# Optimization experiments

Measured on AMD Instinct MI355X. Metric: run time of the kernel, lower is better.

The kernel has to match this reference:

```python
import jax, jax.numpy as jnp
import numpy as np

EPS = 1e-5
BS, NA, NC, NL, NPTS, ED, NG = 1, 900, 6, 4, 13, 256, 8
GD = ED // NG
IMG_W, IMG_H = 704.0, 256.0
FMAP_HW = [(64, 176), (32, 88), (16, 44), (8, 22)]


def _ln(x, g, b):
    m = x.mean(-1, keepdims=True)
    v = ((x - m) ** 2).mean(-1, keepdims=True)
    return (x - m) / jnp.sqrt(v + EPS) * g + b


def _grid_sample(img, grid):
    # img: [N,C,H,W]; grid: [N,P,Q,2] in [-1,1]; bilinear, zeros padding, align_corners=False
    N, C, H, W = img.shape
    gx = jnp.clip((grid[..., 0] + 1.0) * (W * 0.5) - 0.5, -1e4, 1e4)
    gy = jnp.clip((grid[..., 1] + 1.0) * (H * 0.5) - 0.5, -1e4, 1e4)
    x0 = jnp.floor(gx); y0 = jnp.floor(gy)
    wx1 = gx - x0; wy1 = gy - y0; wx0 = 1.0 - wx1; wy0 = 1.0 - wy1
    x0i = x0.astype(jnp.int32); y0i = y0.astype(jnp.int32)
    flat = img.reshape(N, C, H * W)

    def corner(xi, yi, wgt):
        valid = (xi >= 0) & (xi < W) & (yi >= 0) & (yi < H)
        idx = (jnp.clip(yi, 0, H - 1) * W + jnp.clip(xi, 0, W - 1))
        g = jax.vmap(lambda f, i: f[:, i])(flat, idx.reshape(N, -1))  # [N,C,P*Q]
        g = g.reshape(N, C, idx.shape[1], idx.shape[2])
        return g * (wgt * valid)[:, None]

    return (corner(x0i, y0i, wx0 * wy0) + corner(x0i + 1, y0i, wx1 * wy0)
            + corner(x0i, y0i + 1, wx0 * wy1) + corner(x0i + 1, y0i + 1, wx1 * wy1))


def setup_inputs() -> dict:
    key = jax.random.key(0)
    ks = jax.random.split(key, 20)
    d = {}
    d['instance_feature'] = jax.random.normal(ks[0], (BS, NA, ED), jnp.float32)
    xyz = jax.random.normal(ks[1], (BS, NA, 3), jnp.float32) * 1.5
    size = jax.random.normal(ks[2], (BS, NA, 3), jnp.float32) * 0.3
    theta = jax.random.uniform(ks[3], (BS, NA, 1), jnp.float32) * (2.0 * np.pi)
    vel = jax.random.normal(ks[4], (BS, NA, 3), jnp.float32) * 0.1
    d['anchor'] = jnp.concatenate([xyz, size, jnp.sin(theta), jnp.cos(theta), vel], -1)
    d['anchor_embed'] = jax.random.normal(ks[5], (BS, NA, ED), jnp.float32)
    for i, (h, w) in enumerate(FMAP_HW):
        d[f'fmap{i}'] = jax.random.normal(ks[6 + i], (BS, NC, ED, h, w), jnp.float32)
    base = jnp.array([[80., 0., 0., 352.], [0., 80., 0., 128.],
                      [0., 0., 0., 1.], [0., 0., 0., 1.]], jnp.float32)
    proj = jnp.tile(base, (BS, NC, 1, 1))
    proj = proj.at[:, :, :2, :].add(jax.random.normal(ks[10], (BS, NC, 2, 4), jnp.float32) * 2.0)
    d['projection_mat'] = proj
    d['image_wh'] = jnp.broadcast_to(jnp.array([IMG_W, IMG_H], jnp.float32), (BS, NC, 2))
    d['fix_scale'] = jnp.array([[0, 0, 0], [0.45, 0, 0], [-0.45, 0, 0], [0, 0.45, 0],
                                [0, -0.45, 0], [0, 0, 0.45], [0, 0, -0.45]], jnp.float32)

    def w(k, shape):
        return jax.random.normal(k, shape, jnp.float32) * 0.02

    d['lfc_w'] = w(ks[11], (ED, 6 * 3)); d['lfc_b'] = jnp.zeros((18,), jnp.float32)
    d['cam_w1'] = w(ks[12], (12, ED)); d['cam_b1'] = jnp.zeros((ED,), jnp.float32)
    d['cam_g1'] = jnp.ones((ED,), jnp.float32); d['cam_be1'] = jnp.zeros((ED,), jnp.float32)
    d['cam_w2'] = w(ks[13], (ED, ED)); d['cam_b2'] = jnp.zeros((ED,), jnp.float32)
    d['cam_g2'] = jnp.ones((ED,), jnp.float32); d['cam_be2'] = jnp.zeros((ED,), jnp.float32)
    d['wfc_w'] = w(ks[14], (ED, NG * NL * NPTS)); d['wfc_b'] = jnp.zeros((NG * NL * NPTS,), jnp.float32)
    d['op_w'] = w(ks[15], (ED, ED)); d['op_b'] = jnp.zeros((ED,), jnp.float32)
    return d


def reference(instance_feature, anchor, anchor_embed, fmap0, fmap1, fmap2, fmap3,
              projection_mat, image_wh, fix_scale, lfc_w, lfc_b,
              cam_w1, cam_b1, cam_g1, cam_be1, cam_w2, cam_b2, cam_g2, cam_be2,
              wfc_w, wfc_b, op_w, op_b):
    bs, na = instance_feature.shape[:2]
    # ---- keypoint generation ----
    size = jnp.exp(anchor[..., None, 3:6])                       # [bs,na,1,3]
    kp = fix_scale * size                                        # [bs,na,7,3]
    ls = jax.nn.sigmoid(instance_feature @ lfc_w + lfc_b).reshape(bs, na, -1, 3) - 0.5
    kp = jnp.concatenate([kp, ls * size], axis=-2)               # [bs,na,NPTS,3]
    sin, cos = anchor[..., 6:7], anchor[..., 7:8]                # [bs,na,1]
    kx, ky, kz = kp[..., 0], kp[..., 1], kp[..., 2]
    key_points = jnp.stack([cos * kx - sin * ky, sin * kx + cos * ky, kz], -1) \
                 + anchor[..., None, 0:3]                        # [bs,na,NPTS,3]
    # ---- per-cam/level/point group weights ----
    feat = instance_feature + anchor_embed
    cam_in = projection_mat[:, :, :3].reshape(bs, NC, 12)
    h = jax.nn.relu(cam_in @ cam_w1 + cam_b1); h = _ln(h, cam_g1, cam_be1)
    h = jax.nn.relu(h @ cam_w2 + cam_b2); cam_embed = _ln(h, cam_g2, cam_be2)
    f = feat[:, :, None] + cam_embed[:, None]                    # [bs,na,NC,ED]
    wts = (f @ wfc_w + wfc_b).reshape(bs, na, NC * NL * NPTS, NG)
    wts = jax.nn.softmax(wts, axis=-2).reshape(bs, na, NC, NL, NPTS, NG)
    # ---- multi-cam projection + bilinear sampling ----
    pts = jnp.concatenate([key_points, jnp.ones_like(key_points[..., :1])], -1)
    p2d = jnp.einsum('bcij,banj->bcani', projection_mat, pts)    # [bs,NC,na,NPTS,4]
    p2d = p2d[..., :2] / jnp.maximum(p2d[..., 2:3], 1e-5)
    p2d = p2d / image_wh[:, :, None, None]
    grid = (p2d * 2.0 - 1.0).reshape(bs * NC, na, NPTS, 2)
    feats = jnp.stack([_grid_sample(fm.reshape(bs * NC, ED, fm.shape[-2], fm.shape[-1]), grid)
                       for fm in (fmap0, fmap1, fmap2, fmap3)], axis=1)  # [bs*NC,NL,ED,na,NPTS]
    feats = feats.reshape(bs, NC, NL, ED, na, NPTS).transpose(0, 4, 1, 2, 5, 3)  # [bs,na,NC,NL,NPTS,ED]
    # ---- group-weighted fusion over cams & levels, then sum over points ----
    fg = feats.reshape(bs, na, NC, NL, NPTS, NG, GD)
    fused = jnp.einsum('bnclpg,bnclpgd->bnpgd', wts, fg).reshape(bs, na, NPTS, ED)
    fused = fused.sum(axis=2)                                    # [bs,na,ED]
    out = fused @ op_w + op_b
    return jnp.concatenate([out, instance_feature], axis=-1)     # [bs,na,2*ED]
```

## Files before the change

### kernel.cpp

```cpp
#include <hip/hip_runtime.h>
#include <stdint.h>

#define NA 900
#define NC 6
#define NL 4
#define NPTS 13
#define ED 256
#define NG 8
#define LNEPS 1e-5f
#define NTRANS 1416
#define NCOPY 672
#define NSAMP 312
#define LGS 313

struct PIn { const void* p[24]; };

__device__ __forceinline__ float b2f(unsigned short u){
  union { uint32_t i; float f; } v; v.i = ((uint32_t)u)<<16; return v.f;
}
__device__ __forceinline__ unsigned short f2b(float f){
  union { float f; uint32_t i; } v; v.f = f;
  uint32_t r = v.i + 0x7FFFu + ((v.i>>16)&1u);
  return (unsigned short)(r>>16);
}
#define BLO(u) __uint_as_float((u)<<16)
#define BHI(u) __uint_as_float((u)&0xffff0000u)

__device__ __forceinline__ float ldx(const void* p, int i, bool bf){
  return bf ? b2f(((const unsigned short*)p)[i]) : ((const float*)p)[i];
}

__device__ __forceinline__ void gload_lds16(const void* g, void* l){
  __builtin_amdgcn_global_load_lds(
      (const __attribute__((address_space(1))) void*)g,
      (__attribute__((address_space(3))) void*)l, 16, 0, 0);
}

__device__ __forceinline__ bool sniff_bf(const unsigned short* __restrict__ u16){
  int lane = threadIdx.x & 63;
  unsigned short u = u16[2*lane];
  int e = (u>>7)&0xFF;
  int sane = (e>=110 && e<=135) ? 1 : 0;
  #pragma unroll
  for (int m=32;m;m>>=1) sane += __shfl_xor(sane, m);
  return sane >= 48;
}

__device__ __forceinline__ void blockReduce2(float& a, float& b, float* lds){
  #pragma unroll
  for (int m=32;m;m>>=1){ a += __shfl_xor(a,m); b += __shfl_xor(b,m); }
  int w = threadIdx.x>>6;
  if ((threadIdx.x&63)==0){ lds[w]=a; lds[w+4]=b; }
  __syncthreads();
  a = lds[0]+lds[1]+lds[2]+lds[3];
  b = lds[4]+lds[5]+lds[6]+lds[7];
  __syncthreads();
}

__global__ __launch_bounds__(256) void k_init(PIn in,
                                              unsigned short* __restrict__ wfcw_h,
                                              unsigned short* __restrict__ opw_h,
                                              float* __restrict__ Bc){
  const bool bf = sniff_bf((const unsigned short*)in.p[0]);
  const int tid = threadIdx.x;
  int b = blockIdx.x;

  __shared__ float h[ED];
  __shared__ float cE[ED];
  __shared__ float red8[8];
  __shared__ float part[4][64];

  if (b < NCOPY){
    int idx = b*256 + tid;
    if (idx < 106496){
      wfcw_h[idx] = bf ? ((const unsigned short*)in.p[20])[idx]
                       : f2b(((const float*)in.p[20])[idx]);
    } else {
      int j = idx - 106496;
      opw_h[j] = bf ? ((const unsigned short*)in.p[22])[j]
                    : f2b(((const float*)in.p[22])[j]);
    }
    return;
  }
  b -= NCOPY;
  {
    const void* proj = in.p[7];
    const void* w1 = in.p[12]; const void* b1 = in.p[13];
    const void* g1 = in.p[14]; const void* be1 = in.p[15];
    const void* w2 = in.p[16]; const void* b2 = in.p[17];
    const void* g2 = in.p[18]; const void* be2 = in.p[19];
    const void* wfcw = in.p[20]; const void* wfcb = in.p[21];
    const int c = b/7, colt = b - (b/7)*7;
    float ci[12];
    #pragma unroll
    for (int i=0;i<12;i++) ci[i] = ldx(proj, c*16+i, bf);
    float acc = ldx(b1, tid, bf);
    #pragma unroll
    for (int k=0;k<12;k++) acc += ci[k]*ldx(w1, k*ED+tid, bf);
    float x = fmaxf(acc, 0.f);
    float s=x, q=x*x;
    blockReduce2(s,q,red8);
    float mean = s*(1.f/ED), var = q*(1.f/ED)-mean*mean;
    h[tid] = (x-mean)*rsqrtf(var+LNEPS)*ldx(g1,tid,bf) + ldx(be1,tid,bf);
    __syncthreads();
    acc = ldx(b2, tid, bf);
    #pragma unroll 8
    for (int k=0;k<ED;k++) acc += h[k]*ldx(w2, k*ED+tid, bf);
    x = fmaxf(acc,0.f);
    s=x; q=x*x;
    blockReduce2(s,q,red8);
    mean = s*(1.f/ED); var = q*(1.f/ED)-mean*mean;
    cE[tid] = (x-mean)*rsqrtf(var+LNEPS)*ldx(g2,tid,bf) + ldx(be2,tid,bf);
    __syncthreads();
    const int kc = tid>>6, colL = tid&63, col = colt*64+colL;
    float a = 0.f;
    if (col < 416){
      #pragma unroll 8
      for (int k=0;k<64;k++) a += cE[kc*64+k]*ldx(wfcw, (kc*64+k)*416+col, bf);
    }
    part[kc][colL] = a;
    __syncthreads();
    if (kc==0 && col<416)
      Bc[c*416+col] = part[0][colL]+part[1][colL]+part[2][colL]+part[3][colL] + ldx(wfcb,col,bf);
  }
}

__global__ __launch_bounds__(256) void k_work(PIn in,
                                              unsigned short* __restrict__ tf,
                                              const unsigned short* __restrict__ wfcw_h,
                                              const float* __restrict__ Bc,
                                              uint4* __restrict__ gdesc, int* __restrict__ mcnt,
                                              void* __restrict__ outv){
  const bool bf = sniff_bf((const unsigned short*)in.p[0]);
  const int tid = threadIdx.x;
  int b = blockIdx.x;

  __shared__ __align__(16) char smem[32768];

  if (b < NTRANS){
    const int tiles[4] = {44,11,3,1};
    const int HWs[4]   = {11264,2816,704,176};
    const int TFO[4]   = {0,17301504,21626880,22708224};
    int l, local;
    if      (b < 1056){ l=0; local=b;      }
    else if (b < 1320){ l=1; local=b-1056; }
    else if (b < 1392){ l=2; local=b-1320; }
    else              { l=3; local=b-1392; }
    int pt = local % tiles[l]; int rest = local / tiles[l];
    int ct = rest & 3; int c = rest >> 2;
    const int HW = HWs[l];
    const int px0 = pt*256;
    const void* src = in.p[3+l];
    const int j8 = tid & 7;
    const int w8 = tid >> 3;

    int nq = 4;
    while (nq > 1 && px0 + (nq-1)*64 >= HW) nq--;

    if (!bf){
      float* TTf = (float*)smem;
      const int wv = tid >> 6;
      const int ln = tid & 63;
      const int rq = ln >> 4;
      const int g  = ln & 15;

      auto issueph = [&](int q){
        const int pxq = px0 + q*64;
        float* dst0 = TTf + (q&1)*4096;
        #pragma unroll
        for (int i=0;i<4;i++){
          int r   = wv*16 + i*4 + rq;
          int swz = (r>>3) & 7;
          int px  = pxq + 4*(g ^ swz);
          if (px + 4 > HW) px = HW - 4;
          const float* gsrc = (const float*)src + (size_t)(c*ED + ct*64 + r)*HW + px;
          gload_lds16(gsrc, (void*)(dst0 + (wv*16 + i*4)*64));
        }
      };

      issueph(0);
      for (int q=0; q<nq; q++){
        if (q+1 < nq){
          issueph(q+1);
          asm volatile("s_waitcnt vmcnt(4)" ::: "memory");
        } else {
          asm volatile("s_waitcnt vmcnt(0)" ::: "memory");
        }
        __builtin_amdgcn_s_barrier();
        const float* T = TTf + (q&1)*4096;
        #pragma unroll
        for (int p=0;p<2;p++){
          int pxl = p*32 + w8;
          int px  = px0 + q*64 + pxl;
          int s   = 4*((pxl>>2) ^ j8) + (pxl&3);
          if (px < HW){
            unsigned short u[8];
            #pragma unroll
            for (int k=0;k<8;k++)
              u[k] = f2b(T[(j8*8+k)*64 + s]);
            uint4 o;
            o.x = (uint32_t)u[0] | ((uint32_t)u[1]<<16);
            o.y = (uint32_t)u[2] | ((uint32_t)u[3]<<16);
            o.z = (uint32_t)u[4] | ((uint32_t)u[5]<<16);
            o.w = (uint32_t)u[6] | ((uint32_t)u[7]<<16);
            *reinterpret_cast<uint4*>(tf + TFO[l] + (size_t)c*HW*ED + (size_t)px*ED + ct*64 + j8*8) = o;
          }
        }
        __builtin_amdgcn_s_barrier();
      }
      return;
    }
    {
      typedef unsigned short u16tile[64][64];
      u16tile* TT = (u16tile*)smem;
      uint4 v[2][4];
      #pragma unroll
      for (int p=0;p<2;p++){
        int ch = ct*64 + p*32 + w8;
        size_t rowb = (size_t)(c*ED+ch)*HW;
        #pragma unroll
        for (int q=0;q<4;q++){
          int pxs = px0 + q*64 + j8*8;
          v[p][q] = (pxs < HW)
            ? *reinterpret_cast<const uint4*>((const unsigned short*)src + rowb + pxs)
            : make_uint4(0,0,0,0);
        }
      }
      for (int q=0;q<nq;q++){
        const int buf = q & 1;
        #pragma unroll
        for (int p=0;p<2;p++){
          int r = p*32 + w8;
          int g8 = (j8 ^ (r>>3))<<3;
          *reinterpret_cast<uint4*>(&TT[buf][r][g8]) = v[p][q];
        }
        __syncthreads();
        #pragma unroll
        for (int p=0;p<2;p++){
          int pxl = p*32 + w8;
          int px  = px0 + q*64 + pxl;
          int colq = (((pxl>>3) ^ j8)<<3) | (pxl & 7);
          int rb = j8*8;
          unsigned short t0 = TT[buf][rb+0][colq], t1 = TT[buf][rb+1][colq];
          unsigned short t2 = TT[buf][rb+2][colq], t3 = TT[buf][rb+3][colq];
          unsigned short t4 = TT[buf][rb+4][colq], t5 = TT[buf][rb+5][colq];
          unsigned short t6 = TT[buf][rb+6][colq], t7 = TT[buf][rb+7][colq];
          uint4 o;
          o.x = (uint32_t)t0 | ((uint32_t)t1<<16);
          o.y = (uint32_t)t2 | ((uint32_t)t3<<16);
          o.z = (uint32_t)t4 | ((uint32_t)t5<<16);
          o.w = (uint32_t)t6 | ((uint32_t)t7<<16);
          if (px < HW)
            *reinterpret_cast<uint4*>(tf + TFO[l] + (size_t)c*HW*ED + (size_t)px*ED + ct*64 + j8*8) = o;
        }
      }
      return;
    }
  }
  const int n = b - NTRANS;
  float* ifs = (float*)(smem);
  float* fe  = (float*)(smem + 1024);
  float* lg2 = (float*)(smem + 2048);
  float (*kp)[3] = (float (*)[3])(smem + 12160);
  float* sc  = (float*)(smem + 12352);
  float* lsv = (float*)(smem + 12416);
  int*   scnt= (int*)(smem + 12544);

  const void* p_inst = in.p[0];
  const void* p_anc  = in.p[1];
  const void* p_ae   = in.p[2];
  const void* p_proj = in.p[7];
  const void* p_imwh = in.p[8];
  const void* p_fixs = in.p[9];
  const void* p_lw   = in.p[10];
  const void* p_lb   = in.p[11];

  {
    if (tid==0) *scnt = 0;
    float iv = ldx(p_inst, n*ED+tid, bf);
    ifs[tid] = iv;
    fe[tid]  = iv + ldx(p_ae, n*ED+tid, bf);
    if (bf) ((unsigned short*)outv)[n*512+256+tid] = f2b(iv);
    else    ((float*)outv)[n*512+256+tid]          = iv;
    if (tid >= 256-8){
      int t = tid - (256-8);
      if (t < 3)       sc[t] = ldx(p_anc, n*11+t, bf);
      else if (t == 3) sc[3] = ldx(p_anc, n*11+6, bf);
      else if (t == 4) sc[4] = ldx(p_anc, n*11+7, bf);
      else             sc[t] = __expf(ldx(p_anc, n*11+t-2, bf));
    }
  }
  __syncthreads();
  if (tid < 144){
    int d = tid>>3, j = tid&7;
    float a = 0.f;
    #pragma unroll 8
    for (int k=j*32;k<j*32+32;k++) a += ifs[k]*ldx(p_lw, k*18+d, bf);
    a += __shfl_xor(a,1); a += __shfl_xor(a,2); a += __shfl_xor(a,4);
    if (j==0){
      a += ldx(p_lb, d, bf);
      lsv[d] = 1.f/(1.f+__expf(-a)) - 0.5f;
    }
  }
  __syncthreads();
  if (tid < 13){
    float kx,ky,kz;
    if (tid < 7){
      kx = ldx(p_fixs, tid*3+0, bf)*sc[5];
      ky = ldx(p_fixs, tid*3+1, bf)*sc[6];
      kz = ldx(p_fixs, tid*3+2, bf)*sc[7];
    } else {
      int j = tid-7;
      kx = lsv[j*3+0]*sc[5]; ky = lsv[j*3+1]*sc[6]; kz = lsv[j*3+2]*sc[7];
    }
    kp[tid][0] = sc[4]*kx - sc[3]*ky + sc[0];
    kp[tid][1] = sc[3]*kx + sc[4]*ky + sc[1];
    kp[tid][2] = kz + sc[2];
  }
  {
    int col2 = (tid < 160) ? tid+256 : 415;
    float a0 = 0.f, a1 = 0.f;
    #pragma unroll 4
    for (int k=0;k<ED;k++){
      float fv = fe[k];
      a0 += fv*b2f(wfcw_h[k*416+tid]);
      a1 += fv*b2f(wfcw_h[k*416+col2]);
    }
    const int g = tid & 7, rr = tid >> 3;
    const int g2 = col2 & 7, rr2 = col2 >> 3;
    #pragma unroll
    for (int c=0;c<NC;c++){
      lg2[g*LGS + c*52 + rr] = a0 + Bc[c*416+tid];
      if (tid < 160) lg2[g2*LGS + c*52 + rr2] = a1 + Bc[c*416+col2];
    }
  }
  __syncthreads();
  {
    const int g = tid>>5, j = tid&31;
    float v[10]; float mx = -1e30f;
    #pragma unroll
    for (int i=0;i<10;i++){
      int e = j + 32*i;
      float val = -1e30f;
      if (e < NSAMP){ val = lg2[g*LGS + e]; mx = fmaxf(mx, val); }
      v[i] = val;
    }
    #pragma unroll
    for (int mk=16;mk;mk>>=1) mx = fmaxf(mx, __shfl_xor(mx, mk, 32));
    float sum = 0.f;
    #pragma unroll
    for (int i=0;i<10;i++){
      if (j + 32*i < NSAMP){ float ex = __expf(v[i]-mx); v[i] = ex; sum += ex; }
    }
    #pragma unroll
    for (int mk=16;mk;mk>>=1) sum += __shfl_xor(sum, mk, 32);
    float inv = 1.f/sum;
    #pragma unroll
    for (int i=0;i<10;i++){
      int e = j + 32*i;
      if (e < NSAMP) lg2[g*LGS + e] = v[i]*inv;
    }
  }
  __syncthreads();
  #pragma unroll
  for (int pass=0;pass<2;pass++){
    int s = tid + pass*256;
    if (s < NSAMP){
      int c = s/52, rr = s - c*52;
      int l = rr/13, p = rr - l*13;
      float m[12];
      #pragma unroll
      for (int i=0;i<12;i++) m[i] = ldx(p_proj, c*16+i, bf);
      float X=kp[p][0], Y=kp[p][1], Z=kp[p][2];
      float x = m[0]*X + m[1]*Y + m[2]*Z  + m[3];
      float y = m[4]*X + m[5]*Y + m[6]*Z  + m[7];
      float z = m[8]*X + m[9]*Y + m[10]*Z + m[11];
      float d = fmaxf(z, 1e-5f);
      float px = x/(d*ldx(p_imwh, c*2+0, bf)), py = y/(d*ldx(p_imwh, c*2+1, bf));
      const int W = 176>>l, H = 64>>l;
      const int TFO[4] = {0,17301504,21626880,22708224};
      float gx = fminf(fmaxf(px*(float)W - 0.5f, -10000.f), 10000.f);
      float gy = fminf(fmaxf(py*(float)H - 0.5f, -10000.f), 10000.f);
      float xf = floorf(gx), yf = floorf(gy);
      int x0 = (int)xf, y0 = (int)yf;
      float wx1 = gx-xf, wy1 = gy-yf;
      float wx0 = 1.f-wx1, wy0 = 1.f-wy1;
      bool vx0 = (x0>=0)&&(x0<W),   vx1 = (x0+1>=0)&&(x0+1<W);
      bool vy0 = (y0>=0)&&(y0<H),   vy1 = (y0+1>=0)&&(y0+1<H);
      float w00 = (vx0&&vy0) ? wx0*wy0 : 0.f;
      float w10 = (vx1&&vy0) ? wx1*wy0 : 0.f;
      float w01 = (vx0&&vy1) ? wx0*wy1 : 0.f;
      float w11 = (vx1&&vy1) ? wx1*wy1 : 0.f;
      if (w00+w10+w01+w11 != 0.f){
        int cx0 = min(max(x0,0),W-1), cx1 = min(max(x0+1,0),W-1);
        int cy0 = min(max(y0,0),H-1), cy1 = min(max(y0+1,0),H-1);
        uint32_t cam = (uint32_t)TFO[l] + (uint32_t)(c*H*W)*ED;
        uint4 bi, wv;
        bi.x = cam + (uint32_t)(cy0*W+cx0)*ED;
        bi.y = cam + (uint32_t)(cy0*W+cx1)*ED;
        bi.z = cam + (uint32_t)(cy1*W+cx0)*ED;
        bi.w = cam + (uint32_t)(cy1*W+cx1)*ED;
        wv.x = __float_as_uint(w00); wv.y = __float_as_uint(w10);
        wv.z = __float_as_uint(w01); wv.w = __float_as_uint(w11);
        float4 wa = make_float4(lg2[0*LGS+s], lg2[1*LGS+s], lg2[2*LGS+s], lg2[3*LGS+s]);
        float4 wb = make_float4(lg2[4*LGS+s], lg2[5*LGS+s], lg2[6*LGS+s], lg2[7*LGS+s]);
        int slot = atomicAdd(scnt, 1);
        uint4* dst = gdesc + (size_t)(n*NSAMP + slot)*4;
        dst[0] = bi;
        dst[1] = wv;
        dst[2] = *reinterpret_cast<uint4*>(&wa);
        dst[3] = *reinterpret_cast<uint4*>(&wb);
      }
    }
  }
  __syncthreads();
  if (tid==0) mcnt[n] = *scnt;
}

__global__ __launch_bounds__(512, 4) void k_gather(
    const unsigned short* __restrict__ tf,
    const unsigned short* __restrict__ opw_h, const uint4* __restrict__ gdesc,
    const int* __restrict__ mcnt, const void* __restrict__ rawinst,
    const void* __restrict__ opb, void* __restrict__ outv){
  const int n = blockIdx.x, tid = threadIdx.x;
  const bool bf = sniff_bf((const unsigned short*)rawinst);

  __shared__ uint4 ldesc[NSAMP*4];
  __shared__ float red[8][ED+4];
  __shared__ float fu[ED];

  const int m = mcnt[n];
  {
    const uint4* src = gdesc + (size_t)n*NSAMP*4;
    for (int j=tid; j < m*4; j += 512) ldesc[j] = src[j];
  }
  __syncthreads();

  {
    const int strm = tid>>5, lane32 = tid&31;
    const int ch8 = lane32*8, gg = lane32>>2;
    float acc[8] = {0,0,0,0,0,0,0,0};
    int i = strm;
    for (; i + 16 < m; i += 32){
      uint4 biA = ldesc[i*4],      wfA = ldesc[i*4+1];
      uint4 biB = ldesc[(i+16)*4], wfB = ldesc[(i+16)*4+1];
      float wgA = reinterpret_cast<const float*>(&ldesc[i*4+2])[gg];
      float wgB = reinterpret_cast<const float*>(&ldesc[(i+16)*4+2])[gg];
      uint4 a00 = *reinterpret_cast<const uint4*>(tf + biA.x + ch8);
      uint4 a10 = *reinterpret_cast<const uint4*>(tf + biA.y + ch8);
      uint4 a01 = *reinterpret_cast<const uint4*>(tf + biA.z + ch8);
      uint4 a11 = *reinterpret_cast<const uint4*>(tf + biA.w + ch8);
      uint4 b00 = *reinterpret_cast<const uint4*>(tf + biB.x + ch8);
      uint4 b10 = *reinterpret_cast<const uint4*>(tf + biB.y + ch8);
      uint4 b01 = *reinterpret_cast<const uint4*>(tf + biB.z + ch8);
      uint4 b11 = *reinterpret_cast<const uint4*>(tf + biB.w + ch8);
      float pA00 = wgA*__uint_as_float(wfA.x), pA10 = wgA*__uint_as_float(wfA.y);
      float pA01 = wgA*__uint_as_float(wfA.z), pA11 = wgA*__uint_as_float(wfA.w);
      float pB00 = wgB*__uint_as_float(wfB.x), pB10 = wgB*__uint_as_float(wfB.y);
      float pB01 = wgB*__uint_as_float(wfB.z), pB11 = wgB*__uint_as_float(wfB.w);
      acc[0] += pA00*BLO(a00.x)+pA10*BLO(a10.x)+pA01*BLO(a01.x)+pA11*BLO(a11.x)
              + pB00*BLO(b00.x)+pB10*BLO(b10.x)+pB01*BLO(b01.x)+pB11*BLO(b11.x);
      acc[1] += pA00*BHI(a00.x)+pA10*BHI(a10.x)+pA01*BHI(a01.x)+pA11*BHI(a11.x)
              + pB00*BHI(b00.x)+pB10*BHI(b10.x)+pB01*BHI(b01.x)+pB11*BHI(b11.x);
      acc[2] += pA00*BLO(a00.y)+pA10*BLO(a10.y)+pA01*BLO(a01.y)+pA11*BLO(a11.y)
              + pB00*BLO(b00.y)+pB10*BLO(b10.y)+pB01*BLO(b01.y)+pB11*BLO(b11.y);
      acc[3] += pA00*BHI(a00.y)+pA10*BHI(a10.y)+pA01*BHI(a01.y)+pA11*BHI(a11.y)
              + pB00*BHI(b00.y)+pB10*BHI(b10.y)+pB01*BHI(b01.y)+pB11*BHI(b11.y);
      acc[4] += pA00*BLO(a00.z)+pA10*BLO(a10.z)+pA01*BLO(a01.z)+pA11*BLO(a11.z)
              + pB00*BLO(b00.z)+pB10*BLO(b10.z)+pB01*BLO(b01.z)+pB11*BLO(b11.z);
      acc[5] += pA00*BHI(a00.z)+pA10*BHI(a10.z)+pA01*BHI(a01.z)+pA11*BHI(a11.z)
              + pB00*BHI(b00.z)+pB10*BHI(b10.z)+pB01*BHI(b01.z)+pB11*BHI(b11.z);
      acc[6] += pA00*BLO(a00.w)+pA10*BLO(a10.w)+pA01*BLO(a01.w)+pA11*BLO(a11.w)
              + pB00*BLO(b00.w)+pB10*BLO(b10.w)+pB01*BLO(b01.w)+pB11*BLO(b11.w);
      acc[7] += pA00*BHI(a00.w)+pA10*BHI(a10.w)+pA01*BHI(a01.w)+pA11*BHI(a11.w)
              + pB00*BHI(b00.w)+pB10*BHI(b10.w)+pB01*BHI(b01.w)+pB11*BHI(b11.w);
    }
    for (; i < m; i += 16){
      uint4 bi = ldesc[i*4], wf = ldesc[i*4+1];
      float wg = reinterpret_cast<const float*>(&ldesc[i*4+2])[gg];
      uint4 q00 = *reinterpret_cast<const uint4*>(tf + bi.x + ch8);
      uint4 q10 = *reinterpret_cast<const uint4*>(tf + bi.y + ch8);
      uint4 q01 = *reinterpret_cast<const uint4*>(tf + bi.z + ch8);
      uint4 q11 = *reinterpret_cast<const uint4*>(tf + bi.w + ch8);
      float p00 = wg*__uint_as_float(wf.x), p10 = wg*__uint_as_float(wf.y);
      float p01 = wg*__uint_as_float(wf.z), p11 = wg*__uint_as_float(wf.w);
      acc[0] += p00*BLO(q00.x)+p10*BLO(q10.x)+p01*BLO(q01.x)+p11*BLO(q11.x);
      acc[1] += p00*BHI(q00.x)+p10*BHI(q10.x)+p01*BHI(q01.x)+p11*BHI(q11.x);
      acc[2] += p00*BLO(q00.y)+p10*BLO(q10.y)+p01*BLO(q01.y)+p11*BLO(q11.y);
      acc[3] += p00*BHI(q00.y)+p10*BHI(q10.y)+p01*BHI(q01.y)+p11*BHI(q11.y);
      acc[4] += p00*BLO(q00.z)+p10*BLO(q10.z)+p01*BLO(q01.z)+p11*BLO(q11.z);
      acc[5] += p00*BHI(q00.z)+p10*BHI(q10.z)+p01*BHI(q01.z)+p11*BHI(q11.z);
      acc[6] += p00*BLO(q00.w)+p10*BLO(q10.w)+p01*BLO(q01.w)+p11*BLO(q11.w);
      acc[7] += p00*BHI(q00.w)+p10*BHI(q10.w)+p01*BHI(q01.w)+p11*BHI(q11.w);
    }
    #pragma unroll
    for (int j=0;j<8;j++) acc[j] += __shfl_xor(acc[j], 32);
    const int w = tid>>6;
    if ((tid&63) < 32){
      *reinterpret_cast<float4*>(&red[w][ch8])   = make_float4(acc[0],acc[1],acc[2],acc[3]);
      *reinterpret_cast<float4*>(&red[w][ch8+4]) = make_float4(acc[4],acc[5],acc[6],acc[7]);
    }
  }
  __syncthreads();
  if (tid < 256){
    float r = 0.f;
    #pragma unroll
    for (int i=0;i<8;i++) r += red[i][tid];
    fu[tid] = r;
  }
  __syncthreads();
  {
    const int col = tid & 255, half = tid >> 8;
    const int k0 = half*128;
    float a = 0.f;
    #pragma unroll 8
    for (int k=k0;k<k0+128;k++) a += fu[k]*b2f(opw_h[k*ED+col]);
    red[half][col] = a;
  }
  __syncthreads();
  if (tid < 256){
    float v = ldx(opb, tid, bf) + red[0][tid] + red[1][tid];
    if (bf) ((unsigned short*)outv)[n*512+tid] = f2b(v);
    else    ((float*)outv)[n*512+tid]          = v;
  }
}

extern "C" void kernel_launch(void* const* d_in, const int* in_sizes, int n_in,
                              void* d_out, int out_size, void* d_ws, size_t ws_size,
                              hipStream_t stream){
  char* ws = (char*)d_ws;
  size_t off = 0;
  auto alloc = [&](size_t bytes)->char*{
    char* p = ws + off; off += (bytes + 63) & ~size_t(63); return p;
  };
  unsigned short* tf = (unsigned short*)alloc((size_t)22978560*2);
  unsigned short* wfcw_h = (unsigned short*)alloc((size_t)106496*2);
  unsigned short* opw_h  = (unsigned short*)alloc((size_t)65536*2);
  float* Bc     = (float*)alloc((size_t)NC*416*4);
  uint4* gdesc  = (uint4*)alloc((size_t)NA*NSAMP*64);
  int*   mcnt   = (int*)alloc((size_t)NA*4);

  PIn in;
  for (int i=0;i<24;i++) in.p[i] = d_in[i];

  k_init<<<NCOPY + 42, 256, 0, stream>>>(in, wfcw_h, opw_h, Bc);
  k_work<<<NTRANS + NA, 256, 0, stream>>>(in, tf, wfcw_h, Bc, gdesc, mcnt, d_out);
  k_gather<<<NA, 512, 0, stream>>>(tf, opw_h, gdesc, mcnt, d_in[0], d_in[23], d_out);
}
```

Before: 259.2 us.

## Split gather per pyramid level with ticketed cross-block reduction; reorder work blocks

Descriptor generation now buckets samples by pyramid level (78 slots each) and runs in the first blocks of the work kernel, ahead of the transpose blocks. The gather kernel launches four 256-thread blocks per anchor, one per level, instead of one 512-thread block. Each block writes a partial sum to global memory, and the last-arriving block, chosen by an atomic ticket, reduces the partials and does the output projection. This gives more and smaller blocks for better occupancy and load balance, at the cost of partial-buffer traffic, fences and atomics, and a serial 256-deep projection loop in one block per anchor.

```diff
diff --git a/kernel.cpp b/kernel.cpp
--- a/kernel.cpp
+++ b/kernel.cpp
@@ -11,6 +11,7 @@
 #define NTRANS 1416
 #define NCOPY 672
 #define NSAMP 312
+#define CHL 78
 #define LGS 313
 
 struct PIn { const void* p[24]; };
@@ -130,6 +131,7 @@
                                               const unsigned short* __restrict__ wfcw_h,
                                               const float* __restrict__ Bc,
                                               uint4* __restrict__ gdesc, int* __restrict__ mcnt,
+                                              int* __restrict__ ticket,
                                               void* __restrict__ outv){
   const bool bf = sniff_bf((const unsigned short*)in.p[0]);
   const int tid = threadIdx.x;
@@ -137,7 +139,170 @@
 
   __shared__ __align__(16) char smem[32768];
 
-  if (b < NTRANS){
+  if (b < NA){
+    const int n = b;
+    float* ifs = (float*)(smem);
+    float* fe  = (float*)(smem + 1024);
+    float* lg2 = (float*)(smem + 2048);
+    float (*kp)[3] = (float (*)[3])(smem + 12160);
+    float* sc  = (float*)(smem + 12352);
+    float* lsv = (float*)(smem + 12416);
+    int*  scnt4= (int*)(smem + 12544);
+
+    const void* p_inst = in.p[0];
+    const void* p_anc  = in.p[1];
+    const void* p_ae   = in.p[2];
+    const void* p_proj = in.p[7];
+    const void* p_imwh = in.p[8];
+    const void* p_fixs = in.p[9];
+    const void* p_lw   = in.p[10];
+    const void* p_lb   = in.p[11];
+
+    {
+      if (tid < 4) scnt4[tid] = 0;
+      if (tid == 4) ticket[n] = 0;
+      float iv = ldx(p_inst, n*ED+tid, bf);
+      ifs[tid] = iv;
+      fe[tid]  = iv + ldx(p_ae, n*ED+tid, bf);
+      if (bf) ((unsigned short*)outv)[n*512+256+tid] = f2b(iv);
+      else    ((float*)outv)[n*512+256+tid]          = iv;
+      if (tid >= 256-8){
+        int t = tid - (256-8);
+        if (t < 3)       sc[t] = ldx(p_anc, n*11+t, bf);
+        else if (t == 3) sc[3] = ldx(p_anc, n*11+6, bf);
+        else if (t == 4) sc[4] = ldx(p_anc, n*11+7, bf);
+        else             sc[t] = __expf(ldx(p_anc, n*11+t-2, bf));
+      }
+    }
+    __syncthreads();
+    if (tid < 144){
+      int d = tid>>3, j = tid&7;
+      float a = 0.f;
+      #pragma unroll 8
+      for (int k=j*32;k<j*32+32;k++) a += ifs[k]*ldx(p_lw, k*18+d, bf);
+      a += __shfl_xor(a,1); a += __shfl_xor(a,2); a += __shfl_xor(a,4);
+      if (j==0){
+        a += ldx(p_lb, d, bf);
+        lsv[d] = 1.f/(1.f+__expf(-a)) - 0.5f;
+      }
+    }
+    __syncthreads();
+    if (tid < 13){
+      float kx,ky,kz;
+      if (tid < 7){
+        kx = ldx(p_fixs, tid*3+0, bf)*sc[5];
+        ky = ldx(p_fixs, tid*3+1, bf)*sc[6];
+        kz = ldx(p_fixs, tid*3+2, bf)*sc[7];
+      } else {
+        int j = tid-7;
+        kx = lsv[j*3+0]*sc[5]; ky = lsv[j*3+1]*sc[6]; kz = lsv[j*3+2]*sc[7];
+      }
+      kp[tid][0] = sc[4]*kx - sc[3]*ky + sc[0];
+      kp[tid][1] = sc[3]*kx + sc[4]*ky + sc[1];
+      kp[tid][2] = kz + sc[2];
+    }
+    {
+      int col2 = (tid < 160) ? tid+256 : 415;
+      float a0 = 0.f, a1 = 0.f;
+      #pragma unroll 4
+      for (int k=0;k<ED;k++){
+        float fv = fe[k];
+        a0 += fv*b2f(wfcw_h[k*416+tid]);
+        a1 += fv*b2f(wfcw_h[k*416+col2]);
+      }
+      const int g = tid & 7, rr = tid >> 3;
+      const int g2 = col2 & 7, rr2 = col2 >> 3;
+      #pragma unroll
+      for (int c=0;c<NC;c++){
+        lg2[g*LGS + c*52 + rr] = a0 + Bc[c*416+tid];
+        if (tid < 160) lg2[g2*LGS + c*52 + rr2] = a1 + Bc[c*416+col2];
+      }
+    }
+    __syncthreads();
+    {
+      const int g = tid>>5, j = tid&31;
+      float v[10]; float mx = -1e30f;
+      #pragma unroll
+      for (int i=0;i<10;i++){
+        int e = j + 32*i;
+        float val = -1e30f;
+        if (e < NSAMP){ val = lg2[g*LGS + e]; mx = fmaxf(mx, val); }
+        v[i] = val;
+      }
+      #pragma unroll
+      for (int mk=16;mk;mk>>=1) mx = fmaxf(mx, __shfl_xor(mx, mk, 32));
+      float sum = 0.f;
+      #pragma unroll
+      for (int i=0;i<10;i++){
+        if (j + 32*i < NSAMP){ float ex = __expf(v[i]-mx); v[i] = ex; sum += ex; }
+      }
+      #pragma unroll
+      for (int mk=16;mk;mk>>=1) sum += __shfl_xor(sum, mk, 32);
+      float inv = 1.f/sum;
+      #pragma unroll
+      for (int i=0;i<10;i++){
+        int e = j + 32*i;
+        if (e < NSAMP) lg2[g*LGS + e] = v[i]*inv;
+      }
+    }
+    __syncthreads();
+    #pragma unroll
+    for (int pass=0;pass<2;pass++){
+      int s = tid + pass*256;
+      if (s < NSAMP){
+        int c = s/52, rr = s - c*52;
+        int l = rr/13, p = rr - l*13;
+        float m[12];
+        #pragma unroll
+        for (int i=0;i<12;i++) m[i] = ldx(p_proj, c*16+i, bf);
+        float X=kp[p][0], Y=kp[p][1], Z=kp[p][2];
+        float x = m[0]*X + m[1]*Y + m[2]*Z  + m[3];
+        float y = m[4]*X + m[5]*Y + m[6]*Z  + m[7];
+        float z = m[8]*X + m[9]*Y + m[10]*Z + m[11];
+        float d = fmaxf(z, 1e-5f);
+        float px = x/(d*ldx(p_imwh, c*2+0, bf)), py = y/(d*ldx(p_imwh, c*2+1, bf));
+        const int W = 176>>l, H = 64>>l;
+        const int TFO[4] = {0,17301504,21626880,22708224};
+        float gx = fminf(fmaxf(px*(float)W - 0.5f, -10000.f), 10000.f);
+        float gy = fminf(fmaxf(py*(float)H - 0.5f, -10000.f), 10000.f);
+        float xf = floorf(gx), yf = floorf(gy);
+        int x0 = (int)xf, y0 = (int)yf;
+        float wx1 = gx-xf, wy1 = gy-yf;
+        float wx0 = 1.f-wx1, wy0 = 1.f-wy1;
+        bool vx0 = (x0>=0)&&(x0<W),   vx1 = (x0+1>=0)&&(x0+1<W);
+        bool vy0 = (y0>=0)&&(y0<H),   vy1 = (y0+1>=0)&&(y0+1<H);
+        float w00 = (vx0&&vy0) ? wx0*wy0 : 0.f;
+        float w10 = (vx1&&vy0) ? wx1*wy0 : 0.f;
+        float w01 = (vx0&&vy1) ? wx0*wy1 : 0.f;
+        float w11 = (vx1&&vy1) ? wx1*wy1 : 0.f;
+        if (w00+w10+w01+w11 != 0.f){
+          int cx0 = min(max(x0,0),W-1), cx1 = min(max(x0+1,0),W-1);
+          int cy0 = min(max(y0,0),H-1), cy1 = min(max(y0+1,0),H-1);
+          uint32_t cam = (uint32_t)TFO[l] + (uint32_t)(c*H*W)*ED;
+          uint4 bi, wv;
+          bi.x = cam + (uint32_t)(cy0*W+cx0)*ED;
+          bi.y = cam + (uint32_t)(cy0*W+cx1)*ED;
+          bi.z = cam + (uint32_t)(cy1*W+cx0)*ED;
+          bi.w = cam + (uint32_t)(cy1*W+cx1)*ED;
+          wv.x = __float_as_uint(w00); wv.y = __float_as_uint(w10);
+          wv.z = __float_as_uint(w01); wv.w = __float_as_uint(w11);
+          float4 wa = make_float4(lg2[0*LGS+s], lg2[1*LGS+s], lg2[2*LGS+s], lg2[3*LGS+s]);
+          float4 wb = make_float4(lg2[4*LGS+s], lg2[5*LGS+s], lg2[6*LGS+s], lg2[7*LGS+s]);
+          int slot = atomicAdd(&scnt4[l], 1);
+          uint4* dst = gdesc + (size_t)(n*NSAMP + l*CHL + slot)*4;
+          dst[0] = bi;
+          dst[1] = wv;
+          dst[2] = *reinterpret_cast<uint4*>(&wa);
+          dst[3] = *reinterpret_cast<uint4*>(&wb);
+        }
+      }
+    }
+    __syncthreads();
+    if (tid < 4) mcnt[n*4+tid] = scnt4[tid];
+    return;
+  }
+  b -= NA;
+  {
     const int tiles[4] = {44,11,3,1};
     const int HWs[4]   = {11264,2816,704,176};
     const int TFO[4]   = {0,17301504,21626880,22708224};
@@ -257,182 +422,28 @@
       return;
     }
   }
-  const int n = b - NTRANS;
-  float* ifs = (float*)(smem);
-  float* fe  = (float*)(smem + 1024);
-  float* lg2 = (float*)(smem + 2048);
-  float (*kp)[3] = (float (*)[3])(smem + 12160);
-  float* sc  = (float*)(smem + 12352);
-  float* lsv = (float*)(smem + 12416);
-  int*   scnt= (int*)(smem + 12544);
-
-  const void* p_inst = in.p[0];
-  const void* p_anc  = in.p[1];
-  const void* p_ae   = in.p[2];
-  const void* p_proj = in.p[7];
-  const void* p_imwh = in.p[8];
-  const void* p_fixs = in.p[9];
-  const void* p_lw   = in.p[10];
-  const void* p_lb   = in.p[11];
-
-  {
-    if (tid==0) *scnt = 0;
-    float iv = ldx(p_inst, n*ED+tid, bf);
-    ifs[tid] = iv;
-    fe[tid]  = iv + ldx(p_ae, n*ED+tid, bf);
-    if (bf) ((unsigned short*)outv)[n*512+256+tid] = f2b(iv);
-    else    ((float*)outv)[n*512+256+tid]          = iv;
-    if (tid >= 256-8){
-      int t = tid - (256-8);
-      if (t < 3)       sc[t] = ldx(p_anc, n*11+t, bf);
-      else if (t == 3) sc[3] = ldx(p_anc, n*11+6, bf);
-      else if (t == 4) sc[4] = ldx(p_anc, n*11+7, bf);
-      else             sc[t] = __expf(ldx(p_anc, n*11+t-2, bf));
-    }
-  }
-  __syncthreads();
-  if (tid < 144){
-    int d = tid>>3, j = tid&7;
-    float a = 0.f;
-    #pragma unroll 8
-    for (int k=j*32;k<j*32+32;k++) a += ifs[k]*ldx(p_lw, k*18+d, bf);
-    a += __shfl_xor(a,1); a += __shfl_xor(a,2); a += __shfl_xor(a,4);
-    if (j==0){
-      a += ldx(p_lb, d, bf);
-      lsv[d] = 1.f/(1.f+__expf(-a)) - 0.5f;
-    }
-  }
-  __syncthreads();
-  if (tid < 13){
-    float kx,ky,kz;
-    if (tid < 7){
-      kx = ldx(p_fixs, tid*3+0, bf)*sc[5];
-      ky = ldx(p_fixs, tid*3+1, bf)*sc[6];
-      kz = ldx(p_fixs, tid*3+2, bf)*sc[7];
-    } else {
-      int j = tid-7;
-      kx = lsv[j*3+0]*sc[5]; ky = lsv[j*3+1]*sc[6]; kz = lsv[j*3+2]*sc[7];
-    }
-    kp[tid][0] = sc[4]*kx - sc[3]*ky + sc[0];
-    kp[tid][1] = sc[3]*kx + sc[4]*ky + sc[1];
-    kp[tid][2] = kz + sc[2];
-  }
-  {
-    int col2 = (tid < 160) ? tid+256 : 415;
-    float a0 = 0.f, a1 = 0.f;
-    #pragma unroll 4
-    for (int k=0;k<ED;k++){
-      float fv = fe[k];
-      a0 += fv*b2f(wfcw_h[k*416+tid]);
-      a1 += fv*b2f(wfcw_h[k*416+col2]);
-    }
-    const int g = tid & 7, rr = tid >> 3;
-    const int g2 = col2 & 7, rr2 = col2 >> 3;
-    #pragma unroll
-    for (int c=0;c<NC;c++){
-      lg2[g*LGS + c*52 + rr] = a0 + Bc[c*416+tid];
-      if (tid < 160) lg2[g2*LGS + c*52 + rr2] = a1 + Bc[c*416+col2];
-    }
-  }
-  __syncthreads();
-  {
-    const int g = tid>>5, j = tid&31;
-    float v[10]; float mx = -1e30f;
-    #pragma unroll
-    for (int i=0;i<10;i++){
-      int e = j + 32*i;
-      float val = -1e30f;
-      if (e < NSAMP){ val = lg2[g*LGS + e]; mx = fmaxf(mx, val); }
-      v[i] = val;
-    }
-    #pragma unroll
-    for (int mk=16;mk;mk>>=1) mx = fmaxf(mx, __shfl_xor(mx, mk, 32));
-    float sum = 0.f;
-    #pragma unroll
-    for (int i=0;i<10;i++){
-      if (j + 32*i < NSAMP){ float ex = __expf(v[i]-mx); v[i] = ex; sum += ex; }
-    }
-    #pragma unroll
-    for (int mk=16;mk;mk>>=1) sum += __shfl_xor(sum, mk, 32);
-    float inv = 1.f/sum;
-    #pragma unroll
-    for (int i=0;i<10;i++){
-      int e = j + 32*i;
-      if (e < NSAMP) lg2[g*LGS + e] = v[i]*inv;
-    }
-  }
-  __syncthreads();
-  #pragma unroll
-  for (int pass=0;pass<2;pass++){
-    int s = tid + pass*256;
-    if (s < NSAMP){
-      int c = s/52, rr = s - c*52;
-      int l = rr/13, p = rr - l*13;
-      float m[12];
-      #pragma unroll
-      for (int i=0;i<12;i++) m[i] = ldx(p_proj, c*16+i, bf);
-      float X=kp[p][0], Y=kp[p][1], Z=kp[p][2];
-      float x = m[0]*X + m[1]*Y + m[2]*Z  + m[3];
-      float y = m[4]*X + m[5]*Y + m[6]*Z  + m[7];
-      float z = m[8]*X + m[9]*Y + m[10]*Z + m[11];
-      float d = fmaxf(z, 1e-5f);
-      float px = x/(d*ldx(p_imwh, c*2+0, bf)), py = y/(d*ldx(p_imwh, c*2+1, bf));
-      const int W = 176>>l, H = 64>>l;
-      const int TFO[4] = {0,17301504,21626880,22708224};
-      float gx = fminf(fmaxf(px*(float)W - 0.5f, -10000.f), 10000.f);
-      float gy = fminf(fmaxf(py*(float)H - 0.5f, -10000.f), 10000.f);
-      float xf = floorf(gx), yf = floorf(gy);
-      int x0 = (int)xf, y0 = (int)yf;
-      float wx1 = gx-xf, wy1 = gy-yf;
-      float wx0 = 1.f-wx1, wy0 = 1.f-wy1;
-      bool vx0 = (x0>=0)&&(x0<W),   vx1 = (x0+1>=0)&&(x0+1<W);
-      bool vy0 = (y0>=0)&&(y0<H),   vy1 = (y0+1>=0)&&(y0+1<H);
-      float w00 = (vx0&&vy0) ? wx0*wy0 : 0.f;
-      float w10 = (vx1&&vy0) ? wx1*wy0 : 0.f;
-      float w01 = (vx0&&vy1) ? wx0*wy1 : 0.f;
-      float w11 = (vx1&&vy1) ? wx1*wy1 : 0.f;
-      if (w00+w10+w01+w11 != 0.f){
-        int cx0 = min(max(x0,0),W-1), cx1 = min(max(x0+1,0),W-1);
-        int cy0 = min(max(y0,0),H-1), cy1 = min(max(y0+1,0),H-1);
-        uint32_t cam = (uint32_t)TFO[l] + (uint32_t)(c*H*W)*ED;
-        uint4 bi, wv;
-        bi.x = cam + (uint32_t)(cy0*W+cx0)*ED;
-        bi.y = cam + (uint32_t)(cy0*W+cx1)*ED;
-        bi.z = cam + (uint32_t)(cy1*W+cx0)*ED;
-        bi.w = cam + (uint32_t)(cy1*W+cx1)*ED;
-        wv.x = __float_as_uint(w00); wv.y = __float_as_uint(w10);
-        wv.z = __float_as_uint(w01); wv.w = __float_as_uint(w11);
-        float4 wa = make_float4(lg2[0*LGS+s], lg2[1*LGS+s], lg2[2*LGS+s], lg2[3*LGS+s]);
-        float4 wb = make_float4(lg2[4*LGS+s], lg2[5*LGS+s], lg2[6*LGS+s], lg2[7*LGS+s]);
-        int slot = atomicAdd(scnt, 1);
-        uint4* dst = gdesc + (size_t)(n*NSAMP + slot)*4;
-        dst[0] = bi;
-        dst[1] = wv;
-        dst[2] = *reinterpret_cast<uint4*>(&wa);
-        dst[3] = *reinterpret_cast<uint4*>(&wb);
-      }
-    }
-  }
-  __syncthreads();
-  if (tid==0) mcnt[n] = *scnt;
-}
-
-__global__ __launch_bounds__(512, 4) void k_gather(
+}
+
+__global__ __launch_bounds__(256, 6) void k_gather(
     const unsigned short* __restrict__ tf,
     const unsigned short* __restrict__ opw_h, const uint4* __restrict__ gdesc,
     const int* __restrict__ mcnt, const void* __restrict__ rawinst,
-    const void* __restrict__ opb, void* __restrict__ outv){
-  const int n = blockIdx.x, tid = threadIdx.x;
+    const void* __restrict__ opb, float* __restrict__ partial,
+    int* __restrict__ ticket, void* __restrict__ outv){
+  const int bid = blockIdx.x;
+  const int l = bid / NA, n = bid - l*NA;
+  const int tid = threadIdx.x;
   const bool bf = sniff_bf((const unsigned short*)rawinst);
-
-  __shared__ uint4 ldesc[NSAMP*4];
-  __shared__ float red[8][ED+4];
+  const int m = mcnt[n*4+l];
+
+  __shared__ uint4 ldesc[CHL*4];
+  __shared__ float red[4][ED+4];
   __shared__ float fu[ED];
-
-  const int m = mcnt[n];
+  __shared__ int win;
+
   {
-    const uint4* src = gdesc + (size_t)n*NSAMP*4;
-    for (int j=tid; j < m*4; j += 512) ldesc[j] = src[j];
+    const uint4* src = gdesc + (size_t)(n*NSAMP + l*CHL)*4;
+    for (int j=tid; j < m*4; j += 256) ldesc[j] = src[j];
   }
   __syncthreads();
 
@@ -441,11 +452,11 @@
     const int ch8 = lane32*8, gg = lane32>>2;
     float acc[8] = {0,0,0,0,0,0,0,0};
     int i = strm;
-    for (; i + 16 < m; i += 32){
-      uint4 biA = ldesc[i*4],      wfA = ldesc[i*4+1];
-      uint4 biB = ldesc[(i+16)*4], wfB = ldesc[(i+16)*4+1];
+    for (; i + 8 < m; i += 16){
+      uint4 biA = ldesc[i*4],     wfA = ldesc[i*4+1];
+      uint4 biB = ldesc[(i+8)*4], wfB = ldesc[(i+8)*4+1];
       float wgA = reinterpret_cast<const float*>(&ldesc[i*4+2])[gg];
-      float wgB = reinterpret_cast<const float*>(&ldesc[(i+16)*4+2])[gg];
+      float wgB = reinterpret_cast<const float*>(&ldesc[(i+8)*4+2])[gg];
       uint4 a00 = *reinterpret_cast<const uint4*>(tf + biA.x + ch8);
       uint4 a10 = *reinterpret_cast<const uint4*>(tf + biA.y + ch8);
       uint4 a01 = *reinterpret_cast<const uint4*>(tf + biA.z + ch8);
@@ -475,7 +486,7 @@
       acc[7] += pA00*BHI(a00.w)+pA10*BHI(a10.w)+pA01*BHI(a01.w)+pA11*BHI(a11.w)
               + pB00*BHI(b00.w)+pB10*BHI(b10.w)+pB01*BHI(b01.w)+pB11*BHI(b11.w);
     }
-    for (; i < m; i += 16){
+    for (; i < m; i += 8){
       uint4 bi = ldesc[i*4], wf = ldesc[i*4+1];
       float wg = reinterpret_cast<const float*>(&ldesc[i*4+2])[gg];
       uint4 q00 = *reinterpret_cast<const uint4*>(tf + bi.x + ch8);
@@ -502,26 +513,28 @@
     }
   }
   __syncthreads();
-  if (tid < 256){
+  partial[(size_t)(l*NA + n)*ED + tid] = red[0][tid] + red[1][tid] + red[2][tid] + red[3][tid];
+  __threadfence();
+  __syncthreads();
+  if (tid == 0){
+    win = (atomicAdd(&ticket[n], 1) == 3);
+  }
+  __syncthreads();
+  if (!win) return;
+  __threadfence();
+  {
     float r = 0.f;
     #pragma unroll
-    for (int i=0;i<8;i++) r += red[i][tid];
+    for (int sp=0;sp<4;sp++) r += partial[(size_t)(sp*NA + n)*ED + tid];
     fu[tid] = r;
   }
   __syncthreads();
   {
-    const int col = tid & 255, half = tid >> 8;
-    const int k0 = half*128;
-    float a = 0.f;
-    #pragma unroll 8
-    for (int k=k0;k<k0+128;k++) a += fu[k]*b2f(opw_h[k*ED+col]);
-    red[half][col] = a;
-  }
-  __syncthreads();
-  if (tid < 256){
-    float v = ldx(opb, tid, bf) + red[0][tid] + red[1][tid];
-    if (bf) ((unsigned short*)outv)[n*512+tid] = f2b(v);
-    else    ((float*)outv)[n*512+tid]          = v;
+    float a = ldx(opb, tid, bf);
+    #pragma unroll 4
+    for (int k=0;k<ED;k++) a += fu[k]*b2f(opw_h[k*ED+tid]);
+    if (bf) ((unsigned short*)outv)[n*512+tid] = f2b(a);
+    else    ((float*)outv)[n*512+tid]          = a;
   }
 }
 
@@ -538,12 +551,14 @@
   unsigned short* opw_h  = (unsigned short*)alloc((size_t)65536*2);
   float* Bc     = (float*)alloc((size_t)NC*416*4);
   uint4* gdesc  = (uint4*)alloc((size_t)NA*NSAMP*64);
-  int*   mcnt   = (int*)alloc((size_t)NA*4);
+  int*   mcnt   = (int*)alloc((size_t)NA*4*4);
+  int*   ticket = (int*)alloc((size_t)NA*4);
+  float* partial= (float*)alloc((size_t)4*NA*ED*4);
 
   PIn in;
   for (int i=0;i<24;i++) in.p[i] = d_in[i];
 
   k_init<<<NCOPY + 42, 256, 0, stream>>>(in, wfcw_h, opw_h, Bc);
-  k_work<<<NTRANS + NA, 256, 0, stream>>>(in, tf, wfcw_h, Bc, gdesc, mcnt, d_out);
-  k_gather<<<NA, 512, 0, stream>>>(tf, opw_h, gdesc, mcnt, d_in[0], d_in[23], d_out);
-}
+  k_work<<<NA + NTRANS, 256, 0, stream>>>(in, tf, wfcw_h, Bc, gdesc, mcnt, ticket, d_out);
+  k_gather<<<4*NA, 256, 0, stream>>>(tf, opw_h, gdesc, mcnt, d_in[0], d_in[23], partial, ticket, d_out);
+}
```

Measured after the change: 672.3 us. 159% more time.
